# Performance work log

Measured on AMD Instinct MI355X. Metric: run time of the kernel, lower is better.

Reference implementation:

```python
import jax, jax.numpy as jnp
from jax import lax
import numpy as np

SEQ_LEN = 96; PRED_LEN = 96; SIGNAL_LEN = 16; NUM_NODES = 256
EMBED = 128; HIDDEN = 64; K_NN = 8; S_SCALE = 2.0; CHEB_ORDER = 2
MA_K = 3; BATCH = 16
C_FREQ = SIGNAL_LEN // 2 + 1          # 9 rfft bins
M_NODES = NUM_NODES * C_FREQ          # nodes per sample graph


def _sin_posemb(pos, dim):
    half = dim // 2
    freqs = 1.0 / (10000.0 ** (np.arange(half) / half))
    ang = pos[:, None] * freqs[None, :]
    return np.concatenate([np.sin(ang), np.cos(ang)], axis=-1).astype(np.float32)


def setup_inputs():
    key = jax.random.key(0)
    ks = jax.random.split(key, 12)
    x = jax.random.normal(ks[0], (BATCH, SEQ_LEN, NUM_NODES), jnp.float32)
    # Chebyshev (order 2) approx of Haar framelet filters cos(xi/2), sin(xi/2) on [0, pi]
    t = np.linspace(-1.0, 1.0, 201); xi = (t + 1.0) * np.pi / 2.0
    ch = np.polynomial.chebyshev
    approx = np.stack([ch.chebfit(t, np.cos(xi / 2.0), CHEB_ORDER),
                       ch.chebfit(t, np.sin(xi / 2.0), CHEB_ORDER)]).astype(np.float32)
    freq_emb = _sin_posemb(np.arange(C_FREQ, dtype=np.float32) * S_SCALE, EMBED)
    sc = (2.0 / EMBED) ** 0.5
    return dict(
        x=x,
        approx=jnp.asarray(approx),                 # [F=2, K=3]
        theta=jnp.ones((2,), jnp.float32),
        fr_Wr=jax.random.normal(ks[1], (EMBED, EMBED), jnp.float32) * sc,
        fr_Wi=jax.random.normal(ks[2], (EMBED, EMBED), jnp.float32) * sc,
        eo_Wr=jax.random.normal(ks[3], (1, EMBED), jnp.float32) * sc,
        eo_Wi=jax.random.normal(ks[4], (1, EMBED), jnp.float32) * sc,
        freq_emb=jnp.asarray(freq_emb),             # [C, EMBED]
        n1_w=jnp.ones((NUM_NODES,), jnp.float32), n1_b=jnp.zeros((NUM_NODES,), jnp.float32),
        n2_w=jnp.ones((NUM_NODES,), jnp.float32), n2_b=jnp.zeros((NUM_NODES,), jnp.float32),
        W1_w=jax.random.normal(ks[5], (HIDDEN, SEQ_LEN), jnp.float32) * (1.0 / SEQ_LEN ** 0.5),
        W1_b=jnp.zeros((HIDDEN,), jnp.float32),
        W2_w=jax.random.normal(ks[6], (HIDDEN, HIDDEN), jnp.float32) * (1.0 / HIDDEN ** 0.5),
        W2_b=jnp.zeros((HIDDEN,), jnp.float32),
        Wt_w=jax.random.normal(ks[7], (HIDDEN, SEQ_LEN), jnp.float32) * (1.0 / SEQ_LEN ** 0.5),
        Wt_b=jnp.zeros((HIDDEN,), jnp.float32),
        W3_w=jax.random.normal(ks[8], (PRED_LEN, HIDDEN), jnp.float32) * (1.0 / HIDDEN ** 0.5),
        W3_b=jnp.zeros((PRED_LEN,), jnp.float32),
    )


def _clinear(z, Wr, Wi):
    xr, xi = z.real, z.imag
    return lax.complex(xr @ Wr.T - xi @ Wi.T, xr @ Wi.T + xi @ Wr.T)


def _csilu(z):
    return lax.complex(jax.nn.silu(z.real), jax.nn.silu(z.imag))


def _cheb_prop(h, row, col, ew, coeffs):
    # Chebyshev recurrence with A_norm(h) = scatter_add(row, (ew/s) * h[col])
    w = (ew / S_SCALE)[:, None]
    def A(hh):
        return jnp.zeros_like(hh).at[row].add(w * hh[col])
    Tx0 = h
    out = coeffs[0] * Tx0
    Tx1 = -A(Tx0)
    out = out + coeffs[1] * Tx1
    for ki in range(2, CHEB_ORDER + 1):
        Tx2 = -2.0 * A(Tx1) - Tx0
        out = out + coeffs[ki] * Tx2
        Tx0, Tx1 = Tx1, Tx2
    return out


def _knn_one(feat):
    # feat [M, 2] -> symmetrised degree-normalised KNN edges
    sq = jnp.sum(feat * feat, axis=1)
    d2 = sq[:, None] + sq[None, :] - 2.0 * (feat @ feat.T)
    d2 = jnp.where(jnp.eye(M_NODES, dtype=bool), jnp.inf, d2)
    idx = lax.top_k(-d2, K_NN)[1]                      # smallest distances
    src = jnp.repeat(jnp.arange(M_NODES), K_NN)
    dst = idx.reshape(-1)
    r = jnp.concatenate([src, dst])
    c = jnp.concatenate([dst, src])
    deg = jnp.zeros((M_NODES,), jnp.float32).at[r].add(1.0)
    dinv = (deg + 1e-8) ** -0.5
    return r, c, dinv[r] * dinv[c]


def _moving_avg(x):
    pad = MA_K // 2
    front = jnp.repeat(x[:, :1, :], pad, axis=1)
    back = jnp.repeat(x[:, -1:, :], MA_K - 1 - pad, axis=1)
    xp = jnp.concatenate([front, x, back], axis=1)     # (B, T+k-1, N)
    cs = jnp.cumsum(xp, axis=1)
    cs = jnp.concatenate([jnp.zeros_like(cs[:, :1, :]), cs], axis=1)
    return (cs[:, MA_K:, :] - cs[:, :-MA_K, :]) / MA_K  # (B, T, N)


def _inorm(h, w, b):
    mu = jnp.mean(h, axis=-1, keepdims=True)
    var = jnp.mean((h - mu) ** 2, axis=-1, keepdims=True)
    return (h - mu) / jnp.sqrt(var + 1e-5) * w[None, :, None] + b[None, :, None]


def _forward(x, approx, theta, fr_Wr, fr_Wi, eo_Wr, eo_Wi, freq_emb,
             n1_w, n1_b, n2_w, n2_b, W1_w, W1_b, W2_w, W2_b, Wt_w, Wt_b, W3_w, W3_b):
    B, T, N = x.shape
    trend = _moving_avg(x)
    seasonal = x - trend
    S = jnp.fft.rfft(seasonal, n=SIGNAL_LEN, axis=1, norm='ortho')   # (B, C, N) c64
    S_perm = jnp.transpose(S, (0, 2, 1))                             # (B, N, C)
    node_feat = S_perm[..., None] * freq_emb                         # (B, N, C, E) c64
    batch_x = node_feat.reshape(B * M_NODES, EMBED)
    sg = S_perm.reshape(B, M_NODES)
    feat = lax.stop_gradient(jnp.stack([sg.real, sg.imag], axis=-1))  # (B, M, 2)
    rs, cs_, ews = jax.vmap(_knn_one)(feat)
    off = (jnp.arange(B) * M_NODES)[:, None]
    row = (rs + off).reshape(-1)
    col = (cs_ + off).reshape(-1)
    ew = ews.reshape(-1)
    # framelet layer: sum of F filtered Chebyshev propagations
    acc = jnp.zeros_like(batch_x)
    for i in range(approx.shape[0]):
        acc = acc + theta[i] * _cheb_prop(batch_x, row, col, ew, approx[i])
    h = _csilu(_clinear(acc, fr_Wr, fr_Wi))
    S_out = _clinear(h, eo_Wr, eo_Wi).reshape(B, N, C_FREQ)
    H = jnp.fft.irfft(jnp.transpose(S_out, (0, 2, 1)), n=SEQ_LEN, axis=1, norm='ortho')
    H = jnp.transpose(H, (0, 2, 1))                                  # (B, N, T)
    H = jax.nn.silu(_inorm(H, n1_w, n1_b))
    H = H @ W1_w.T + W1_b
    H = jax.nn.silu(_inorm(H, n2_w, n2_b))
    H = H @ W2_w.T + W2_b
    trend_emb = jnp.transpose(trend, (0, 2, 1)) @ Wt_w.T + Wt_b
    return (H + trend_emb) @ W3_w.T + W3_b                           # (B, N, pred_len)


def reference(x, approx, theta, fr_Wr, fr_Wi, eo_Wr, eo_Wi, freq_emb,
              n1_w, n1_b, n2_w, n2_b, W1_w, W1_b, W2_w, W2_b, Wt_w, Wt_b, W3_w, W3_b):
    return _forward(x, approx, theta, fr_Wr, fr_Wi, eo_Wr, eo_Wi, freq_emb,
                    n1_w, n1_b, n2_w, n2_b, W1_w, W1_b, W2_w, W2_b, Wt_w, Wt_b, W3_w, W3_b)
```

## Files before the change

### kernel.cpp

```cpp
#include <hip/hip_runtime.h>
#include <math.h>
#include <float.h>

#define BATCH 16
#define SEQ 96
#define NNODE 256
#define CFREQ 9
#define MNODE (NNODE * CFREQ)
#define BM (BATCH * MNODE)
#define KNN 8
#define EMBED 128
#define HIDDEN 64
#define TN (SEQ * NNODE)
#define KCAP 64
#define NBLK (BM / 256)
#define HROWS 4

__constant__ float COS16[16] = {
    1.0f, 0.9238795325112867f, 0.7071067811865476f, 0.3826834323650898f,
    0.0f, -0.3826834323650898f, -0.7071067811865476f, -0.9238795325112867f,
    -1.0f, -0.9238795325112867f, -0.7071067811865476f, -0.3826834323650898f,
    0.0f, 0.3826834323650898f, 0.7071067811865476f, 0.9238795325112867f};
__constant__ float SIN16[16] = {
    0.0f, 0.3826834323650898f, 0.7071067811865476f, 0.9238795325112867f,
    1.0f, 0.9238795325112867f, 0.7071067811865476f, 0.3826834323650898f,
    0.0f, -0.3826834323650898f, -0.7071067811865476f, -0.9238795325112867f,
    -1.0f, -0.9238795325112867f, -0.7071067811865476f, -0.3826834323650898f};

static __device__ __forceinline__ float silu_f(float x) {
    return x / (1.0f + expf(-x));
}

static __device__ __forceinline__ float rank_h(float2 fj, float xi2, float yi2) {
    float sqj = __fmaf_rn(fj.y, fj.y, __fmul_rn(fj.x, fj.x));
    return __fmaf_rn(xi2, fj.x, __fmaf_rn(yi2, fj.y, sqj));
}

__global__ void trend_kernel(const float* __restrict__ x, float* __restrict__ trend) {
    int gid = blockIdx.x * blockDim.x + threadIdx.x;
    if (gid >= BATCH * TN) return;
    int b = gid / TN;
    int rem = gid - b * TN;
    int t = rem / NNODE;
    int n = rem - t * NNODE;
    int tm = t > 0 ? t - 1 : 0;
    int tp = t < SEQ - 1 ? t + 1 : SEQ - 1;
    const float* xb = x + b * TN;
    float v = (xb[tm * NNODE + n] + xb[t * NNODE + n] + xb[tp * NNODE + n]) * (1.0f / 3.0f);
    trend[gid] = v;
}

__global__ void fft_kernel(const float* __restrict__ x, const float* __restrict__ trend,
                           float* __restrict__ S) {
    int gid = blockIdx.x * blockDim.x + threadIdx.x;
    if (gid >= BM) return;
    int b = gid / MNODE;
    int m = gid - b * MNODE;
    int n = m / CFREQ;
    int c = m - n * CFREQ;
    const float* xb = x + b * TN + n;
    const float* tb = trend + b * TN + n;
    float re = 0.0f, im = 0.0f;
    #pragma unroll
    for (int t = 0; t < 16; ++t) {
        float s = xb[t * NNODE] - tb[t * NNODE];
        int k = (c * t) & 15;
        re += s * COS16[k];
        im -= s * SIN16[k];
    }
    S[gid * 2 + 0] = re * 0.25f;
    S[gid * 2 + 1] = im * 0.25f;
}

__global__ void __launch_bounds__(256, 8) knn_kernel(const float* __restrict__ S,
                                                     int* __restrict__ idx, int* __restrict__ cnt) {
    __shared__ float2 f[MNODE];
    __shared__ unsigned long long kbuf[4][KCAP];
    int b = blockIdx.y;
    int tid = threadIdx.x;
    for (int t = tid; t < MNODE; t += 256) {
        f[t] = make_float2(S[(b * MNODE + t) * 2 + 0], S[(b * MNODE + t) * 2 + 1]);
    }
    __syncthreads();
    int wave = tid >> 6, lane = tid & 63;
    int i = blockIdx.x * 4 + wave;
    float2 fi = f[i];
    float xi2 = __fmul_rn(-2.0f, fi.x), yi2 = __fmul_rn(-2.0f, fi.y);
    int lane_i = __builtin_amdgcn_readfirstlane(i & 63);
    int k_i    = __builtin_amdgcn_readfirstlane(i >> 6);

    float h[36];
    float mymin = FLT_MAX;
    #pragma unroll
    for (int k = 0; k < 36; ++k) {
        int j = lane + (k << 6);
        float hh = rank_h(f[j], xi2, yi2);
        if (k == k_i && lane == lane_i) hh = FLT_MAX;
        h[k] = hh;
        mymin = fminf(mymin, hh);
    }
    float g = mymin;
    g = fminf(g, __shfl_xor(g, 1, 64));
    g = fminf(g, __shfl_xor(g, 2, 64));
    g = fminf(g, __shfl_xor(g, 4, 64));
    float T = g;
    T = fmaxf(T, __shfl_xor(T, 8, 64));
    T = fmaxf(T, __shfl_xor(T, 16, 64));
    T = fmaxf(T, __shfl_xor(T, 32, 64));
    unsigned long long* mybuf = kbuf[wave];
    const unsigned long long lmask = (1ull << lane) - 1ull;
    int total = 0;
    #pragma unroll
    for (int k = 0; k < 36; ++k) {
        bool pred = h[k] <= T;
        unsigned long long mask = __ballot(pred);
        if (pred) {
            int pos = total + (int)__popcll(mask & lmask);
            if (pos < KCAP) {
                unsigned int bits = __float_as_uint(h[k]);
                if (bits == 0x80000000u) bits = 0u;
                unsigned int s = bits ^ (unsigned int)(((int)bits >> 31) | 0x80000000);
                mybuf[pos] = ((unsigned long long)s << 32) | (unsigned int)(lane + (k << 6));
            }
        }
        total += (int)__popcll(mask);
    }

    if (total >= KNN && total <= KCAP) {
        int padded = (total + 7) & ~7;
        if (lane < padded - total) mybuf[total + lane] = ~0ull;
        for (int p = lane; p < total; p += 64) {
            unsigned long long mykey = mybuf[p];
            int rank = 0;
            for (int q = 0; q < padded; q += 8) {
                const ulonglong2* bp = (const ulonglong2*)&mybuf[q];
                ulonglong2 a = bp[0], b2 = bp[1], c2 = bp[2], d2 = bp[3];
                rank += (int)(a.x  < mykey) + (int)(a.y  < mykey)
                      + (int)(b2.x < mykey) + (int)(b2.y < mykey)
                      + (int)(c2.x < mykey) + (int)(c2.y < mykey)
                      + (int)(d2.x < mykey) + (int)(d2.y < mykey);
            }
            if (rank < KNN) {
                int j = (int)(unsigned int)(mykey & 0xFFFFFFFFull);
                idx[(b * MNODE + i) * KNN + rank] = j;
                atomicAdd(&cnt[b * MNODE + j], 1);
            }
        }
    } else {
        const unsigned long long SENT = ~0ull;
        unsigned long long k0 = SENT, k1 = SENT, k2 = SENT, k3 = SENT,
                           k4 = SENT, k5 = SENT, k6 = SENT, k7 = SENT;
        #pragma unroll
        for (int k = 0; k < 36; ++k) {
            unsigned int bits = __float_as_uint(h[k]);
            if (bits == 0x80000000u) bits = 0u;
            unsigned int s = bits ^ (unsigned int)(((int)bits >> 31) | 0x80000000);
            unsigned long long key = ((unsigned long long)s << 32) | (unsigned int)(lane + (k << 6));
            if (key < k7) {
                k7 = key;
                if (k7 < k6) { unsigned long long t = k6; k6 = k7; k7 = t; }
                if (k6 < k5) { unsigned long long t = k5; k5 = k6; k6 = t; }
                if (k5 < k4) { unsigned long long t = k4; k4 = k5; k5 = t; }
                if (k4 < k3) { unsigned long long t = k3; k3 = k4; k4 = t; }
                if (k3 < k2) { unsigned long long t = k2; k2 = k3; k3 = t; }
                if (k2 < k1) { unsigned long long t = k1; k1 = k2; k2 = t; }
                if (k1 < k0) { unsigned long long t = k0; k0 = k1; k1 = t; }
            }
        }
        unsigned long long mywin = 0;
        #pragma unroll
        for (int r = 0; r < KNN; ++r) {
            unsigned long long hh = k0;
            #pragma unroll
            for (int off = 32; off > 0; off >>= 1) {
                unsigned long long o = __shfl_xor(hh, off, 64);
                if (o < hh) hh = o;
            }
            if (lane == r) mywin = hh;
            if (k0 == hh) {
                k0 = k1; k1 = k2; k2 = k3; k3 = k4; k4 = k5; k5 = k6; k6 = k7; k7 = SENT;
            }
        }
        if (lane < KNN) {
            int j = (int)(unsigned int)(mywin & 0xFFFFFFFFull);
            idx[(b * MNODE + i) * KNN + lane] = j;
            atomicAdd(&cnt[b * MNODE + j], 1);
        }
    }
}

__global__ void __launch_bounds__(256) dinv_scanblk_kernel(
    const int* __restrict__ cnt, const float* __restrict__ S,
    float* __restrict__ dinv, float* __restrict__ PS, int* __restrict__ bsum) {
    __shared__ int wsum[4];
    int tid = threadIdx.x;
    int gid = blockIdx.x * 256 + tid;
    int c = cnt[gid];
    float deg = (float)(KNN + c);
    float dv = 1.0f / sqrtf(deg + 1e-8f);
    dinv[gid] = dv;
    PS[gid * 2 + 0] = dv * S[gid * 2 + 0];
    PS[gid * 2 + 1] = dv * S[gid * 2 + 1];
    int s = c;
    #pragma unroll
    for (int off = 32; off > 0; off >>= 1) s += __shfl_down(s, off, 64);
    if ((tid & 63) == 0) wsum[tid >> 6] = s;
    __syncthreads();
    if (tid == 0) bsum[blockIdx.x] = wsum[0] + wsum[1] + wsum[2] + wsum[3];
}

__global__ void __launch_bounds__(256) scan_apply_kernel(const int* __restrict__ cnt,
                                                         const int* __restrict__ bsum,
                                                         int* __restrict__ offs) {
    __shared__ int wsum[4];
    __shared__ int sbase[4];
    int tid = threadIdx.x;
    int lane = tid & 63, wv = tid >> 6;
    int bb = 0;
    if (tid < NBLK && tid < (int)blockIdx.x) bb = bsum[tid];
    #pragma unroll
    for (int off = 32; off > 0; off >>= 1) bb += __shfl_down(bb, off, 64);
    if (lane == 0) sbase[wv] = bb;
    int gid = blockIdx.x * 256 + tid;
    int v = cnt[gid];
    int x = v;
    #pragma unroll
    for (int off = 1; off < 64; off <<= 1) {
        int y = __shfl_up(x, off, 64);
        if (lane >= off) x += y;
    }
    if (lane == 63) wsum[wv] = x;
    __syncthreads();
    int base = sbase[0] + sbase[1] + sbase[2] + sbase[3];
    for (int w = 0; w < wv; ++w) base += wsum[w];
    offs[gid] = base + x - v;
}

__global__ void fill_kernel(const int* __restrict__ idx, const int* __restrict__ offs,
                            int* __restrict__ fptr, int* __restrict__ rev) {
    int gid = blockIdx.x * blockDim.x + threadIdx.x;
    if (gid >= BM * KNN) return;
    int b = gid / (MNODE * KNN);
    int rem = gid - b * (MNODE * KNN);
    int i = rem / KNN;
    int gj = b * MNODE + idx[gid];
    int pos = atomicAdd(&fptr[gj], 1);
    rev[offs[gj] + pos] = b * MNODE + i;
}

__global__ void __launch_bounds__(256) gather1_kernel(
    const int* __restrict__ idx, const int* __restrict__ offs, const int* __restrict__ cnt,
    const int* __restrict__ rev, const float* __restrict__ dinv, const float* __restrict__ PS,
    float* __restrict__ zA) {
    int gid = blockIdx.x * blockDim.x + threadIdx.x;
    if (gid >= BM * 4) return;
    int gi = gid >> 2;
    int q = gid & 3;
    int c0 = (q == 0) ? 0 : (1 + 2 * q);
    int nc = (q == 0) ? 3 : 2;
    int b = gi / MNODE;
    float a0 = 0.0f, a1 = 0.0f, a2 = 0.0f, a3 = 0.0f, a4 = 0.0f, a5 = 0.0f;
    #pragma unroll
    for (int k = 0; k < KNN; ++k) {
        int gj = b * MNODE + idx[gi * KNN + k];
        int rel = gj % CFREQ - c0;
        float2 p = ((const float2*)PS)[gj];
        bool t0 = (rel == 0), t1 = (rel == 1), t2 = (rel == 2) && (nc == 3);
        a0 += t0 ? p.x : 0.0f;  a1 += t0 ? p.y : 0.0f;
        a2 += t1 ? p.x : 0.0f;  a3 += t1 ? p.y : 0.0f;
        a4 += t2 ? p.x : 0.0f;  a5 += t2 ? p.y : 0.0f;
    }
    int o = offs[gi], e = o + cnt[gi];
    for (int p_ = o; p_ < e; ++p_) {
        int gk = rev[p_];
        int rel = gk % CFREQ - c0;
        float2 p = ((const float2*)PS)[gk];
        bool t0 = (rel == 0), t1 = (rel == 1), t2 = (rel == 2) && (nc == 3);
        a0 += t0 ? p.x : 0.0f;  a1 += t0 ? p.y : 0.0f;
        a2 += t1 ? p.x : 0.0f;  a3 += t1 ? p.y : 0.0f;
        a4 += t2 ? p.x : 0.0f;  a5 += t2 ? p.y : 0.0f;
    }
    float s = dinv[gi] * 0.5f;
    zA[(gi * CFREQ + c0 + 0) * 2 + 0] = s * a0;
    zA[(gi * CFREQ + c0 + 0) * 2 + 1] = s * a1;
    zA[(gi * CFREQ + c0 + 1) * 2 + 0] = s * a2;
    zA[(gi * CFREQ + c0 + 1) * 2 + 1] = s * a3;
    if (nc == 3) {
        zA[(gi * CFREQ + c0 + 2) * 2 + 0] = s * a4;
        zA[(gi * CFREQ + c0 + 2) * 2 + 1] = s * a5;
    }
}

__global__ void __launch_bounds__(256) gather2_kernel(
    const int* __restrict__ idx, const int* __restrict__ offs, const int* __restrict__ cnt,
    const int* __restrict__ rev, const float* __restrict__ dinv, const float* __restrict__ zA,
    float* __restrict__ zB) {
    int gid = blockIdx.x * blockDim.x + threadIdx.x;
    if (gid >= BM * 4) return;
    int gi = gid >> 2;
    int q = gid & 3;
    int c0 = (q == 0) ? 0 : (1 + 2 * q);
    int nc = (q == 0) ? 3 : 2;
    int b = gi / MNODE;
    float acc[6];
    #pragma unroll
    for (int k = 0; k < 6; ++k) acc[k] = 0.0f;
    float di = dinv[gi] * 0.5f;
    #pragma unroll
    for (int k = 0; k < KNN; ++k) {
        int gj = b * MNODE + idx[gi * KNN + k];
        float w = di * dinv[gj];
        const float2* za = (const float2*)(zA + gj * 2 * CFREQ) + c0;
        #pragma unroll
        for (int c = 0; c < 3; ++c) {
            if (c < nc) {
                float2 v = za[c];
                acc[2 * c + 0] += w * v.x;
                acc[2 * c + 1] += w * v.y;
            }
        }
    }
    int o = offs[gi], e = o + cnt[gi];
    for (int p = o; p < e; ++p) {
        int gk = rev[p];
        float w = di * dinv[gk];
        const float2* za = (const float2*)(zA + gk * 2 * CFREQ) + c0;
        #pragma unroll
        for (int c = 0; c < 3; ++c) {
            if (c < nc) {
                float2 v = za[c];
                acc[2 * c + 0] += w * v.x;
                acc[2 * c + 1] += w * v.y;
            }
        }
    }
    #pragma unroll
    for (int c = 0; c < 3; ++c) {
        if (c < nc) {
            zB[(gi * CFREQ + c0 + c) * 2 + 0] = acc[2 * c + 0];
            zB[(gi * CFREQ + c0 + c) * 2 + 1] = acc[2 * c + 1];
        }
    }
}

__global__ void fe_kernel(const float* __restrict__ femb, const float* __restrict__ Wr,
                          const float* __restrict__ Wi, float* __restrict__ FE) {
    int gid = blockIdx.x * blockDim.x + threadIdx.x;
    if (gid >= CFREQ * EMBED) return;
    int c = gid / EMBED;
    int e = gid - c * EMBED;
    float ar = 0.0f, ai = 0.0f;
    for (int k = 0; k < EMBED; ++k) {
        float f = femb[c * EMBED + k];
        ar += f * Wr[e * EMBED + k];
        ai += f * Wi[e * EMBED + k];
    }
    FE[gid * 2 + 0] = ar;
    FE[gid * 2 + 1] = ai;
}

__global__ void __launch_bounds__(256) rowproj_kernel(
    const float* __restrict__ S, const float* __restrict__ zA, const float* __restrict__ zB,
    const float* __restrict__ FE, const float* __restrict__ eoWr, const float* __restrict__ eoWi,
    const float* __restrict__ theta, const float* __restrict__ approx,
    float* __restrict__ Sout) {
    int wave = threadIdx.x >> 6;
    int lane = threadIdx.x & 63;
    int r = blockIdx.x * 4 + wave;
    if (r >= BM) return;
    float a0 = theta[0] * approx[0] + theta[1] * approx[3];
    float a1 = theta[0] * approx[1] + theta[1] * approx[4];
    float a2 = theta[0] * approx[2] + theta[1] * approx[5];
    float ca = a0 - a2, cb = -a1, cc = 2.0f * a2;
    int cr = r % CFREQ;
    float sr = S[r * 2 + 0], si = S[r * 2 + 1];
    int e1 = lane + 64;
    float ur0 = 0.0f, ui0 = 0.0f, ur1 = 0.0f, ui1 = 0.0f;
    #pragma unroll
    for (int c = 0; c < CFREQ; ++c) {
        float zr = cb * zA[(r * CFREQ + c) * 2 + 0] + cc * zB[(r * CFREQ + c) * 2 + 0];
        float zi = cb * zA[(r * CFREQ + c) * 2 + 1] + cc * zB[(r * CFREQ + c) * 2 + 1];
        if (c == cr) { zr += ca * sr; zi += ca * si; }
        float fr0 = FE[(c * EMBED + lane) * 2 + 0], fi0 = FE[(c * EMBED + lane) * 2 + 1];
        float fr1 = FE[(c * EMBED + e1) * 2 + 0],  fi1 = FE[(c * EMBED + e1) * 2 + 1];
        ur0 += zr * fr0 - zi * fi0;  ui0 += zr * fi0 + zi * fr0;
        ur1 += zr * fr1 - zi * fi1;  ui1 += zr * fi1 + zi * fr1;
    }
    float hr0 = silu_f(ur0), hi0 = silu_f(ui0);
    float hr1 = silu_f(ur1), hi1 = silu_f(ui1);
    float wr0 = eoWr[lane], wi0 = eoWi[lane], wr1 = eoWr[e1], wi1 = eoWi[e1];
    float p = hr0 * wr0 - hi0 * wi0 + hr1 * wr1 - hi1 * wi1;
    float q = hr0 * wi0 + hi0 * wr0 + hr1 * wi1 + hi1 * wr1;
    #pragma unroll
    for (int off = 32; off > 0; off >>= 1) {
        p += __shfl_down(p, off, 64);
        q += __shfl_down(q, off, 64);
    }
    if (lane == 0) {
        Sout[r * 2 + 0] = p;
        Sout[r * 2 + 1] = q;
    }
}

__global__ void __launch_bounds__(256) head_kernel(
    const float* __restrict__ Sout, const float* __restrict__ trend,
    const float* __restrict__ n1w, const float* __restrict__ n1b,
    const float* __restrict__ n2w, const float* __restrict__ n2b,
    const float* __restrict__ W1w, const float* __restrict__ W1b,
    const float* __restrict__ W2w, const float* __restrict__ W2b,
    const float* __restrict__ Wtw, const float* __restrict__ Wtb,
    const float* __restrict__ W3w, const float* __restrict__ W3b,
    float* __restrict__ out) {
    __shared__ float tabc[96], tabs[96];
    __shared__ float srow[HROWS][18];
    __shared__ float tbuf[HROWS][96];
    __shared__ float hraw[HROWS][96];
    __shared__ float sH[HROWS][96];
    __shared__ float h2[HROWS][64];
    __shared__ float s3[HROWS][64];
    __shared__ float red[HROWS][2];
    __shared__ float wbuf[6240];
    int tid = threadIdx.x;
    int wave = tid >> 6, lane = tid & 63;
    int bn0 = blockIdx.x * HROWS;
    if (tid < 96) {
        double a = 6.283185307179586476925286766559 * (double)tid / 96.0;
        tabc[tid] = (float)cos(a);
        tabs[tid] = (float)sin(a);
    }
    for (int i = tid; i < HROWS * 96; i += 256) {
        int g = i / 96, t = i - g * 96;
        int bn = bn0 + g;
        tbuf[g][t] = trend[(bn >> 8) * TN + t * NNODE + (bn & 255)];
    }
    if (tid < HROWS * 18) {
        int g = tid / 18, k = tid - g * 18;
        srow[g][k] = Sout[(bn0 + g) * 18 + k];
    }
    __syncthreads();
    for (int i = tid; i < HROWS * 96; i += 256) {
        int g = i / 96, t = i - g * 96;
        float acc = srow[g][0];
        #pragma unroll
        for (int c = 1; c < CFREQ; ++c) {
            int k = (c * t) % 96;
            acc += 2.0f * (srow[g][2 * c] * tabc[k] - srow[g][2 * c + 1] * tabs[k]);
        }
        hraw[g][t] = acc * 0.10206207261596575f;
    }
    __syncthreads();
    {
        float v = hraw[wave][lane] + ((lane < 32) ? hraw[wave][64 + lane] : 0.0f);
        #pragma unroll
        for (int off = 32; off > 0; off >>= 1) v += __shfl_down(v, off, 64);
        if (lane == 0) red[wave][0] = v * (1.0f / 96.0f);
    }
    __syncthreads();
    {
        float mu = red[wave][0];
        float d0 = hraw[wave][lane] - mu;
        float v = d0 * d0;
        if (lane < 32) { float d1 = hraw[wave][64 + lane] - mu; v += d1 * d1; }
        #pragma unroll
        for (int off = 32; off > 0; off >>= 1) v += __shfl_down(v, off, 64);
        if (lane == 0) red[wave][1] = v * (1.0f / 96.0f);
    }
    __syncthreads();
    for (int i = tid; i < HROWS * 96; i += 256) {
        int g = i / 96, t = i - g * 96;
        int n = (bn0 + g) & 255;
        float xn = (hraw[g][t] - red[g][0]) / sqrtf(red[g][1] + 1e-5f) * n1w[n] + n1b[n];
        sH[g][t] = silu_f(xn);
    }
    for (int i = tid; i < HIDDEN * 96; i += 256) {
        int rr = i / 96;
        wbuf[rr * 97 + (i - rr * 96)] = W1w[i];
    }
    __syncthreads();
    float v1;
    {
        float acc = W1b[lane];
        #pragma unroll 8
        for (int t = 0; t < 96; ++t) acc += sH[wave][t] * wbuf[lane * 97 + t];
        v1 = acc;
    }
    {
        float s = v1;
        #pragma unroll
        for (int off = 32; off > 0; off >>= 1) s += __shfl_down(s, off, 64);
        s = __shfl(s, 0, 64);
        float mu2 = s * (1.0f / 64.0f);
        float d = v1 - mu2;
        float vs = d * d;
        #pragma unroll
        for (int off = 32; off > 0; off >>= 1) vs += __shfl_down(vs, off, 64);
        vs = __shfl(vs, 0, 64);
        float var2 = vs * (1.0f / 64.0f);
        int n = (bn0 + wave) & 255;
        float xn = (v1 - mu2) / sqrtf(var2 + 1e-5f) * n2w[n] + n2b[n];
        h2[wave][lane] = silu_f(xn);
    }
    __syncthreads();
    for (int i = tid; i < HIDDEN * HIDDEN; i += 256) {
        wbuf[(i >> 6) * 65 + (i & 63)] = W2w[i];
    }
    __syncthreads();
    float v3;
    {
        float acc = W2b[lane];
        #pragma unroll 8
        for (int h = 0; h < 64; ++h) acc += h2[wave][h] * wbuf[lane * 65 + h];
        v3 = acc;
    }
    __syncthreads();
    for (int i = tid; i < HIDDEN * 96; i += 256) {
        int rr = i / 96;
        wbuf[rr * 97 + (i - rr * 96)] = Wtw[i];
    }
    __syncthreads();
    {
        float acc = Wtb[lane];
        #pragma unroll 8
        for (int t = 0; t < 96; ++t) acc += tbuf[wave][t] * wbuf[lane * 97 + t];
        s3[wave][lane] = v3 + acc;
    }
    __syncthreads();
    for (int i = tid; i < 96 * HIDDEN; i += 256) {
        wbuf[(i >> 6) * 65 + (i & 63)] = W3w[i];
    }
    __syncthreads();
    for (int i = tid; i < HROWS * 96; i += 256) {
        int g = i / 96, t = i - g * 96;
        float acc = W3b[t];
        #pragma unroll 8
        for (int h = 0; h < 64; ++h) acc += s3[g][h] * wbuf[t * 65 + h];
        out[(bn0 + g) * 96 + t] = acc;
    }
}

extern "C" void kernel_launch(void* const* d_in, const int* in_sizes, int n_in,
                              void* d_out, int out_size, void* d_ws, size_t ws_size,
                              hipStream_t stream) {
    const float* x     = (const float*)d_in[0];
    const float* approx= (const float*)d_in[1];
    const float* theta = (const float*)d_in[2];
    const float* frWr  = (const float*)d_in[3];
    const float* frWi  = (const float*)d_in[4];
    const float* eoWr  = (const float*)d_in[5];
    const float* eoWi  = (const float*)d_in[6];
    const float* femb  = (const float*)d_in[7];
    const float* n1w   = (const float*)d_in[8];
    const float* n1b   = (const float*)d_in[9];
    const float* n2w   = (const float*)d_in[10];
    const float* n2b   = (const float*)d_in[11];
    const float* W1w   = (const float*)d_in[12];
    const float* W1b   = (const float*)d_in[13];
    const float* W2w   = (const float*)d_in[14];
    const float* W2b   = (const float*)d_in[15];
    const float* Wtw   = (const float*)d_in[16];
    const float* Wtb   = (const float*)d_in[17];
    const float* W3w   = (const float*)d_in[18];
    const float* W3b   = (const float*)d_in[19];
    float* out = (float*)d_out;

    char* ws = (char*)d_ws;
    size_t off = 0;
    auto alloc = [&](size_t bytes) -> void* {
        void* p = ws + off;
        off = (off + bytes + 255) & ~(size_t)255;
        return p;
    };
    float* trend = (float*)alloc((size_t)BATCH * TN * 4);
    float* S     = (float*)alloc((size_t)BM * 2 * 4);
    int*   idx   = (int*)  alloc((size_t)BM * KNN * 4);
    float* dinv  = (float*)alloc((size_t)BM * 4);
    float* PS    = (float*)alloc((size_t)BM * 2 * 4);
    float* FE    = (float*)alloc((size_t)CFREQ * EMBED * 2 * 4);
    float* Sout  = (float*)alloc((size_t)BM * 2 * 4);
    int*   offs  = (int*)  alloc((size_t)BM * 4);
    int*   rev   = (int*)  alloc((size_t)BM * KNN * 4);
    float* zA    = (float*)alloc((size_t)BM * CFREQ * 2 * 4);
    float* zB    = (float*)alloc((size_t)BM * CFREQ * 2 * 4);
    int*   bsum  = (int*)  alloc((size_t)NBLK * 4);
    char*  zbase = ws + off;
    int*   cnt   = (int*)  alloc((size_t)BM * 4);
    int*   fptr  = (int*)  alloc((size_t)BM * 4);
    size_t zbytes = (size_t)(ws + off - zbase);

    hipMemsetAsync(zbase, 0, zbytes, stream);

    trend_kernel<<<(BATCH * TN + 255) / 256, 256, 0, stream>>>(x, trend);
    fft_kernel<<<(BM + 255) / 256, 256, 0, stream>>>(x, trend, S);
    knn_kernel<<<dim3(MNODE / 4, BATCH), 256, 0, stream>>>(S, idx, cnt);
    dinv_scanblk_kernel<<<NBLK, 256, 0, stream>>>(cnt, S, dinv, PS, bsum);
    scan_apply_kernel<<<NBLK, 256, 0, stream>>>(cnt, bsum, offs);
    fill_kernel<<<(BM * KNN + 255) / 256, 256, 0, stream>>>(idx, offs, fptr, rev);
    gather1_kernel<<<(BM * 4 + 255) / 256, 256, 0, stream>>>(idx, offs, cnt, rev, dinv, PS, zA);
    gather2_kernel<<<(BM * 4 + 255) / 256, 256, 0, stream>>>(idx, offs, cnt, rev, dinv, zA, zB);
    fe_kernel<<<(CFREQ * EMBED + 255) / 256, 256, 0, stream>>>(femb, frWr, frWi, FE);
    rowproj_kernel<<<BM / 4, 256, 0, stream>>>(S, zA, zB, FE, eoWr, eoWi, theta, approx, Sout);
    head_kernel<<<BATCH * NNODE / HROWS, 256, 0, stream>>>(Sout, trend, n1w, n1b, n2w, n2b,
                                                           W1w, W1b, W2w, W2b, Wtw, Wtb, W3w, W3b, out);
}
```

Before: 260.3 us.

## Fuse trend and FFT prep, widen gather parallelism, double head rows per block

Trend and the 16-point DFT are merged into one kernel that stages x tiles in shared memory, which drops a launch and the trend re-read. The two gather kernels now use one thread per (node, frequency) instead of grouping 2-3 frequencies per thread, giving more threads and contiguous output writes at the cost of repeating the index and neighbour-list traversal for every frequency. The head kernel processes 8 rows per 512-thread block, so each weight matrix is staged once for twice as many rows.

```diff
diff --git a/kernel.cpp b/kernel.cpp
--- a/kernel.cpp
+++ b/kernel.cpp
@@ -14,7 +14,8 @@
 #define TN (SEQ * NNODE)
 #define KCAP 64
 #define NBLK (BM / 256)
-#define HROWS 4
+#define HROWS 8
+#define PN 64
 
 __constant__ float COS16[16] = {
     1.0f, 0.9238795325112867f, 0.7071067811865476f, 0.3826834323650898f,
@@ -36,40 +37,44 @@
     return __fmaf_rn(xi2, fj.x, __fmaf_rn(yi2, fj.y, sqj));
 }
 
-__global__ void trend_kernel(const float* __restrict__ x, float* __restrict__ trend) {
-    int gid = blockIdx.x * blockDim.x + threadIdx.x;
-    if (gid >= BATCH * TN) return;
-    int b = gid / TN;
-    int rem = gid - b * TN;
-    int t = rem / NNODE;
-    int n = rem - t * NNODE;
-    int tm = t > 0 ? t - 1 : 0;
-    int tp = t < SEQ - 1 ? t + 1 : SEQ - 1;
+__global__ void __launch_bounds__(256) prep_kernel(const float* __restrict__ x,
+                                                   float* __restrict__ trend,
+                                                   float* __restrict__ S) {
+    __shared__ float xs[96][PN];
+    __shared__ float ss[16][PN];
+    int b = blockIdx.y;
+    int n0 = blockIdx.x * PN;
+    int tid = threadIdx.x;
     const float* xb = x + b * TN;
-    float v = (xb[tm * NNODE + n] + xb[t * NNODE + n] + xb[tp * NNODE + n]) * (1.0f / 3.0f);
-    trend[gid] = v;
-}
-
-__global__ void fft_kernel(const float* __restrict__ x, const float* __restrict__ trend,
-                           float* __restrict__ S) {
-    int gid = blockIdx.x * blockDim.x + threadIdx.x;
-    if (gid >= BM) return;
-    int b = gid / MNODE;
-    int m = gid - b * MNODE;
-    int n = m / CFREQ;
-    int c = m - n * CFREQ;
-    const float* xb = x + b * TN + n;
-    const float* tb = trend + b * TN + n;
-    float re = 0.0f, im = 0.0f;
-    #pragma unroll
-    for (int t = 0; t < 16; ++t) {
-        float s = xb[t * NNODE] - tb[t * NNODE];
-        int k = (c * t) & 15;
-        re += s * COS16[k];
-        im -= s * SIN16[k];
-    }
-    S[gid * 2 + 0] = re * 0.25f;
-    S[gid * 2 + 1] = im * 0.25f;
+    for (int i = tid; i < 96 * PN; i += 256) {
+        int t = i >> 6, n = i & 63;
+        xs[t][n] = xb[t * NNODE + n0 + n];
+    }
+    __syncthreads();
+    float* tb = trend + b * TN;
+    for (int i = tid; i < 96 * PN; i += 256) {
+        int t = i >> 6, n = i & 63;
+        int tm = t > 0 ? t - 1 : 0;
+        int tp = t < SEQ - 1 ? t + 1 : SEQ - 1;
+        float v = (xs[tm][n] + xs[t][n] + xs[tp][n]) * (1.0f / 3.0f);
+        tb[t * NNODE + n0 + n] = v;
+        if (t < 16) ss[t][n] = xs[t][n] - v;
+    }
+    __syncthreads();
+    for (int o = tid; o < PN * CFREQ; o += 256) {
+        int n = o / 9, c = o - n * 9;
+        float re = 0.0f, im = 0.0f;
+        #pragma unroll
+        for (int t = 0; t < 16; ++t) {
+            float s = ss[t][n];
+            int k = (c * t) & 15;
+            re += s * COS16[k];
+            im -= s * SIN16[k];
+        }
+        int m = (n0 + n) * CFREQ + c;
+        S[(b * MNODE + m) * 2 + 0] = re * 0.25f;
+        S[(b * MNODE + m) * 2 + 1] = im * 0.25f;
+    }
 }
 
 __global__ void __launch_bounds__(256, 8) knn_kernel(const float* __restrict__ S,
@@ -253,42 +258,30 @@
     const int* __restrict__ rev, const float* __restrict__ dinv, const float* __restrict__ PS,
     float* __restrict__ zA) {
     int gid = blockIdx.x * blockDim.x + threadIdx.x;
-    if (gid >= BM * 4) return;
-    int gi = gid >> 2;
-    int q = gid & 3;
-    int c0 = (q == 0) ? 0 : (1 + 2 * q);
-    int nc = (q == 0) ? 3 : 2;
+    if (gid >= BM * CFREQ) return;
+    int gi = gid / CFREQ;
+    int c = gid - gi * CFREQ;
     int b = gi / MNODE;
-    float a0 = 0.0f, a1 = 0.0f, a2 = 0.0f, a3 = 0.0f, a4 = 0.0f, a5 = 0.0f;
+    float ax = 0.0f, ay = 0.0f;
     #pragma unroll
     for (int k = 0; k < KNN; ++k) {
         int gj = b * MNODE + idx[gi * KNN + k];
-        int rel = gj % CFREQ - c0;
+        bool m = (gj % CFREQ) == c;
         float2 p = ((const float2*)PS)[gj];
-        bool t0 = (rel == 0), t1 = (rel == 1), t2 = (rel == 2) && (nc == 3);
-        a0 += t0 ? p.x : 0.0f;  a1 += t0 ? p.y : 0.0f;
-        a2 += t1 ? p.x : 0.0f;  a3 += t1 ? p.y : 0.0f;
-        a4 += t2 ? p.x : 0.0f;  a5 += t2 ? p.y : 0.0f;
+        ax += m ? p.x : 0.0f;
+        ay += m ? p.y : 0.0f;
     }
     int o = offs[gi], e = o + cnt[gi];
     for (int p_ = o; p_ < e; ++p_) {
         int gk = rev[p_];
-        int rel = gk % CFREQ - c0;
+        bool m = (gk % CFREQ) == c;
         float2 p = ((const float2*)PS)[gk];
-        bool t0 = (rel == 0), t1 = (rel == 1), t2 = (rel == 2) && (nc == 3);
-        a0 += t0 ? p.x : 0.0f;  a1 += t0 ? p.y : 0.0f;
-        a2 += t1 ? p.x : 0.0f;  a3 += t1 ? p.y : 0.0f;
-        a4 += t2 ? p.x : 0.0f;  a5 += t2 ? p.y : 0.0f;
+        ax += m ? p.x : 0.0f;
+        ay += m ? p.y : 0.0f;
     }
     float s = dinv[gi] * 0.5f;
-    zA[(gi * CFREQ + c0 + 0) * 2 + 0] = s * a0;
-    zA[(gi * CFREQ + c0 + 0) * 2 + 1] = s * a1;
-    zA[(gi * CFREQ + c0 + 1) * 2 + 0] = s * a2;
-    zA[(gi * CFREQ + c0 + 1) * 2 + 1] = s * a3;
-    if (nc == 3) {
-        zA[(gi * CFREQ + c0 + 2) * 2 + 0] = s * a4;
-        zA[(gi * CFREQ + c0 + 2) * 2 + 1] = s * a5;
-    }
+    zA[gid * 2 + 0] = s * ax;
+    zA[gid * 2 + 1] = s * ay;
 }
 
 __global__ void __launch_bounds__(256) gather2_kernel(
@@ -296,51 +289,30 @@
     const int* __restrict__ rev, const float* __restrict__ dinv, const float* __restrict__ zA,
     float* __restrict__ zB) {
     int gid = blockIdx.x * blockDim.x + threadIdx.x;
-    if (gid >= BM * 4) return;
-    int gi = gid >> 2;
-    int q = gid & 3;
-    int c0 = (q == 0) ? 0 : (1 + 2 * q);
-    int nc = (q == 0) ? 3 : 2;
+    if (gid >= BM * CFREQ) return;
+    int gi = gid / CFREQ;
+    int c = gid - gi * CFREQ;
     int b = gi / MNODE;
-    float acc[6];
-    #pragma unroll
-    for (int k = 0; k < 6; ++k) acc[k] = 0.0f;
+    float ax = 0.0f, ay = 0.0f;
     float di = dinv[gi] * 0.5f;
     #pragma unroll
     for (int k = 0; k < KNN; ++k) {
         int gj = b * MNODE + idx[gi * KNN + k];
         float w = di * dinv[gj];
-        const float2* za = (const float2*)(zA + gj * 2 * CFREQ) + c0;
-        #pragma unroll
-        for (int c = 0; c < 3; ++c) {
-            if (c < nc) {
-                float2 v = za[c];
-                acc[2 * c + 0] += w * v.x;
-                acc[2 * c + 1] += w * v.y;
-            }
-        }
+        float2 v = ((const float2*)zA)[gj * CFREQ + c];
+        ax += w * v.x;
+        ay += w * v.y;
     }
     int o = offs[gi], e = o + cnt[gi];
     for (int p = o; p < e; ++p) {
         int gk = rev[p];
         float w = di * dinv[gk];
-        const float2* za = (const float2*)(zA + gk * 2 * CFREQ) + c0;
-        #pragma unroll
-        for (int c = 0; c < 3; ++c) {
-            if (c < nc) {
-                float2 v = za[c];
-                acc[2 * c + 0] += w * v.x;
-                acc[2 * c + 1] += w * v.y;
-            }
-        }
-    }
-    #pragma unroll
-    for (int c = 0; c < 3; ++c) {
-        if (c < nc) {
-            zB[(gi * CFREQ + c0 + c) * 2 + 0] = acc[2 * c + 0];
-            zB[(gi * CFREQ + c0 + c) * 2 + 1] = acc[2 * c + 1];
-        }
-    }
+        float2 v = ((const float2*)zA)[gk * CFREQ + c];
+        ax += w * v.x;
+        ay += w * v.y;
+    }
+    zB[gid * 2 + 0] = ax;
+    zB[gid * 2 + 1] = ay;
 }
 
 __global__ void fe_kernel(const float* __restrict__ femb, const float* __restrict__ Wr,
@@ -402,7 +374,7 @@
     }
 }
 
-__global__ void __launch_bounds__(256) head_kernel(
+__global__ void __launch_bounds__(512) head_kernel(
     const float* __restrict__ Sout, const float* __restrict__ trend,
     const float* __restrict__ n1w, const float* __restrict__ n1b,
     const float* __restrict__ n2w, const float* __restrict__ n2b,
@@ -428,7 +400,7 @@
         tabc[tid] = (float)cos(a);
         tabs[tid] = (float)sin(a);
     }
-    for (int i = tid; i < HROWS * 96; i += 256) {
+    for (int i = tid; i < HROWS * 96; i += 512) {
         int g = i / 96, t = i - g * 96;
         int bn = bn0 + g;
         tbuf[g][t] = trend[(bn >> 8) * TN + t * NNODE + (bn & 255)];
@@ -438,7 +410,7 @@
         srow[g][k] = Sout[(bn0 + g) * 18 + k];
     }
     __syncthreads();
-    for (int i = tid; i < HROWS * 96; i += 256) {
+    for (int i = tid; i < HROWS * 96; i += 512) {
         int g = i / 96, t = i - g * 96;
         float acc = srow[g][0];
         #pragma unroll
@@ -466,13 +438,13 @@
         if (lane == 0) red[wave][1] = v * (1.0f / 96.0f);
     }
     __syncthreads();
-    for (int i = tid; i < HROWS * 96; i += 256) {
+    for (int i = tid; i < HROWS * 96; i += 512) {
         int g = i / 96, t = i - g * 96;
         int n = (bn0 + g) & 255;
         float xn = (hraw[g][t] - red[g][0]) / sqrtf(red[g][1] + 1e-5f) * n1w[n] + n1b[n];
         sH[g][t] = silu_f(xn);
     }
-    for (int i = tid; i < HIDDEN * 96; i += 256) {
+    for (int i = tid; i < HIDDEN * 96; i += 512) {
         int rr = i / 96;
         wbuf[rr * 97 + (i - rr * 96)] = W1w[i];
     }
@@ -501,7 +473,7 @@
         h2[wave][lane] = silu_f(xn);
     }
     __syncthreads();
-    for (int i = tid; i < HIDDEN * HIDDEN; i += 256) {
+    for (int i = tid; i < HIDDEN * HIDDEN; i += 512) {
         wbuf[(i >> 6) * 65 + (i & 63)] = W2w[i];
     }
     __syncthreads();
@@ -513,7 +485,7 @@
         v3 = acc;
     }
     __syncthreads();
-    for (int i = tid; i < HIDDEN * 96; i += 256) {
+    for (int i = tid; i < HIDDEN * 96; i += 512) {
         int rr = i / 96;
         wbuf[rr * 97 + (i - rr * 96)] = Wtw[i];
     }
@@ -525,11 +497,11 @@
         s3[wave][lane] = v3 + acc;
     }
     __syncthreads();
-    for (int i = tid; i < 96 * HIDDEN; i += 256) {
+    for (int i = tid; i < 96 * HIDDEN; i += 512) {
         wbuf[(i >> 6) * 65 + (i & 63)] = W3w[i];
     }
     __syncthreads();
-    for (int i = tid; i < HROWS * 96; i += 256) {
+    for (int i = tid; i < HROWS * 96; i += 512) {
         int g = i / 96, t = i - g * 96;
         float acc = W3b[t];
         #pragma unroll 8
@@ -589,16 +561,15 @@
 
     hipMemsetAsync(zbase, 0, zbytes, stream);
 
-    trend_kernel<<<(BATCH * TN + 255) / 256, 256, 0, stream>>>(x, trend);
-    fft_kernel<<<(BM + 255) / 256, 256, 0, stream>>>(x, trend, S);
+    prep_kernel<<<dim3(NNODE / PN, BATCH), 256, 0, stream>>>(x, trend, S);
     knn_kernel<<<dim3(MNODE / 4, BATCH), 256, 0, stream>>>(S, idx, cnt);
     dinv_scanblk_kernel<<<NBLK, 256, 0, stream>>>(cnt, S, dinv, PS, bsum);
     scan_apply_kernel<<<NBLK, 256, 0, stream>>>(cnt, bsum, offs);
     fill_kernel<<<(BM * KNN + 255) / 256, 256, 0, stream>>>(idx, offs, fptr, rev);
-    gather1_kernel<<<(BM * 4 + 255) / 256, 256, 0, stream>>>(idx, offs, cnt, rev, dinv, PS, zA);
-    gather2_kernel<<<(BM * 4 + 255) / 256, 256, 0, stream>>>(idx, offs, cnt, rev, dinv, zA, zB);
+    gather1_kernel<<<(BM * CFREQ + 255) / 256, 256, 0, stream>>>(idx, offs, cnt, rev, dinv, PS, zA);
+    gather2_kernel<<<(BM * CFREQ + 255) / 256, 256, 0, stream>>>(idx, offs, cnt, rev, dinv, zA, zB);
     fe_kernel<<<(CFREQ * EMBED + 255) / 256, 256, 0, stream>>>(femb, frWr, frWi, FE);
     rowproj_kernel<<<BM / 4, 256, 0, stream>>>(S, zA, zB, FE, eoWr, eoWi, theta, approx, Sout);
-    head_kernel<<<BATCH * NNODE / HROWS, 256, 0, stream>>>(Sout, trend, n1w, n1b, n2w, n2b,
+    head_kernel<<<BATCH * NNODE / HROWS, 512, 0, stream>>>(Sout, trend, n1w, n1b, n2w, n2b,
                                                            W1w, W1b, W2w, W2b, Wtw, Wtb, W3w, W3b, out);
 }
```

Result: no change. 260.9 us (+0.2%).
